# Kernel tuning notes

Hardware: AMD Instinct MI355X
Metric: run time of the kernel (lower is better)

The kernel has to match this reference:

```python
import jax, jax.numpy as jnp
import numpy as np
import math

D_MODEL = 2048
K = 64
W = 512              # window_size
STRIDE = W // 2      # = 256
EMA_ALPHA = 0.9
N_RETRIEVE = 8
EPS = 1e-12


def _build_cheby(k, w):
    # cheby_mat[k, n] = cos(k * arccos(t_n)), t_n = cos(pi*(2n+1)/(2w))
    ns = np.arange(w, dtype=np.float64)
    t = np.cos(np.pi * (2 * ns + 1) / (2 * w))
    ks = np.arange(k, dtype=np.float64)
    return jnp.asarray(np.cos(ks[:, None] * np.arccos(t)[None, :]), dtype=jnp.float32)


def setup_inputs() -> dict:
    key = jax.random.key(0)
    ks = jax.random.split(key, 5)
    B, S = 2, 8192
    scan_out = jax.random.normal(ks[0], (B, S, D_MODEL), dtype=jnp.float32)
    buf = jax.random.normal(ks[1], (W, D_MODEL), dtype=jnp.float32)  # pre-filled circular buffer
    # unit-modulus random-phase complex roles: r_k[d] = exp(i*theta)
    phases = jax.random.uniform(ks[2], (K, D_MODEL), dtype=jnp.float32) * (2.0 * math.pi)
    roles_real = jnp.cos(phases)
    roles_imag = jnp.sin(phases)
    w_bands = 1.0 / (jnp.arange(K, dtype=jnp.float32) + 1.0)  # w_init = 1/(k+1)
    retrieve_proj_w = jax.random.normal(ks[3], (D_MODEL, D_MODEL), dtype=jnp.float32) * 0.02
    inject_gate = jnp.zeros((1,), dtype=jnp.float32)
    cheby_mat = _build_cheby(K, W)
    return dict(scan_out=scan_out, buf=buf, roles_real=roles_real, roles_imag=roles_imag,
                w_bands=w_bands, retrieve_proj_w=retrieve_proj_w, inject_gate=inject_gate,
                cheby_mat=cheby_mat)


def reference(scan_out, buf, roles_real, roles_imag, w_bands, retrieve_proj_w, inject_gate, cheby_mat):
    S = scan_out.shape[1]
    h_mean = scan_out.mean(axis=0)                      # [S, D] batch-mean like torch code
    n_chunks = S // STRIDE
    chunks = h_mean.reshape(n_chunks, STRIDE, D_MODEL)  # each chunk triggers one bind

    init = (buf, jnp.int32(0),
            jnp.zeros((K, D_MODEL), jnp.float32),   # c_past
            jnp.zeros((D_MODEL,), jnp.float32),     # V_mem_real
            jnp.zeros((D_MODEL,), jnp.float32),     # V_mem_imag
            jnp.zeros((K,), jnp.float32),           # _coeff_norms (EMA)
            jnp.zeros((K,), jnp.float32))           # spectral_delta

    def step(carry, chunk):
        b, pos, c_past, vr, vi, cnorms, _ = carry
        # circular-buffer write of `stride` tokens starting at pos
        b = jax.lax.dynamic_update_slice(b, chunk, (pos, 0))
        pos = (pos + STRIDE) % W
        order = (jnp.arange(W, dtype=jnp.int32) + pos) % W   # oldest-first reorder
        data = b[order]                                      # [W, D]
        # Chebyshev coefficients: c = (2/W) * cheby_mat @ data, c0 halved
        coeffs = (2.0 / W) * (cheby_mat @ data)              # [K, D]
        coeffs = coeffs.at[0].multiply(0.5)
        # HRR-normalized bind into holographic memory via EMA
        norms = jnp.maximum(jnp.linalg.norm(coeffs, axis=-1, keepdims=True), EPS)
        cn = coeffs / norms
        cnorms = EMA_ALPHA * cnorms + (1.0 - EMA_ALPHA) * norms[:, 0]
        vr = EMA_ALPHA * vr + (1.0 - EMA_ALPHA) * (cn * roles_real).sum(axis=0)
        vi = EMA_ALPHA * vi + (1.0 - EMA_ALPHA) * (cn * roles_imag).sum(axis=0)
        # spectral delta vs previous window's coefficients
        delta = jnp.linalg.norm(coeffs - c_past, axis=-1)    # [K]
        return (b, pos, coeffs, vr, vi, cnorms, delta), None

    (b, pos, c_now, vr, vi, cnorms, delta), _ = jax.lax.scan(step, init, chunks)

    # retrieve: unbind top-J bands by spectral delta, denormalize, weight, project
    _, top = jax.lax.top_k(delta, N_RETRIEVE)                # [J]
    rr = roles_real[top]
    ri = roles_imag[top]
    retrieved = (vr[None, :] * rr + vi[None, :] * ri) * jnp.maximum(cnorms[top], EPS)[:, None]  # [J, D]
    weights = jax.nn.softplus(w_bands[top])                  # [J]
    ctx = (weights[:, None] * retrieved).sum(axis=0)         # [D]
    out = (ctx @ retrieve_proj_w.T) * jax.nn.sigmoid(inject_gate[0])  # [D]
    return out, delta, vr, vi
```

## Files before the change

kernel.cpp:

```cpp
#include <hip/hip_runtime.h>
#include <math.h>

#define D_MODEL 2048
#define KB_ 64
#define NCHUNK 32

typedef __bf16 bf16;
typedef __attribute__((ext_vector_type(8))) __bf16 bf16x8;
typedef __attribute__((ext_vector_type(4))) __bf16 bf16x4;
typedef __attribute__((ext_vector_type(4))) float f32x4;

#define OFF_COEFFS 0
#define OFF_NSQ    (32 * 64 * 2048)
#define OFF_NORMS  (OFF_NSQ + 32 * 64 * 32)
#define OFF_VR     (OFF_NORMS + 2048)
#define OFF_VI     (OFF_VR + 2048)
#define OFF_DSQ    (OFF_VI + 2048)

__device__ __forceinline__ void load_stage(
    const float* __restrict__ scan, const float* __restrict__ buf,
    int c, int nb, int n0, int dcol, float4* ra, float4* rb)
{
  if (c == 0 && nb < 4) {
    const float* bp = buf + (256 + nb * 64 + n0) * 2048 + dcol;
#pragma unroll
    for (int i = 0; i < 4; ++i) { ra[i] = *(const float4*)(bp + i * 2048); rb[i] = ra[i]; }
  } else {
    const float* p0 = scan + (c * 256 - 256 + nb * 64 + n0) * 2048 + dcol;
    const float* p1 = p0 + 8192 * 2048;
#pragma unroll
    for (int i = 0; i < 4; ++i) {
      ra[i] = *(const float4*)(p0 + i * 2048);
      rb[i] = *(const float4*)(p1 + i * 2048);
    }
  }
}

__device__ __forceinline__ void store_stage(
    bf16* Bsbuf, int n0, int d4, const float4* ra, const float4* rb)
{
  float4 m0 = make_float4(0.5f * (ra[0].x + rb[0].x), 0.5f * (ra[0].y + rb[0].y),
                          0.5f * (ra[0].z + rb[0].z), 0.5f * (ra[0].w + rb[0].w));
  float4 m1 = make_float4(0.5f * (ra[1].x + rb[1].x), 0.5f * (ra[1].y + rb[1].y),
                          0.5f * (ra[1].z + rb[1].z), 0.5f * (ra[1].w + rb[1].w));
  float4 m2 = make_float4(0.5f * (ra[2].x + rb[2].x), 0.5f * (ra[2].y + rb[2].y),
                          0.5f * (ra[2].z + rb[2].z), 0.5f * (ra[2].w + rb[2].w));
  float4 m3 = make_float4(0.5f * (ra[3].x + rb[3].x), 0.5f * (ra[3].y + rb[3].y),
                          0.5f * (ra[3].z + rb[3].z), 0.5f * (ra[3].w + rb[3].w));
  bf16x4 e0 = {(bf16)m0.x, (bf16)m1.x, (bf16)m2.x, (bf16)m3.x};
  bf16x4 e1 = {(bf16)m0.y, (bf16)m1.y, (bf16)m2.y, (bf16)m3.y};
  bf16x4 e2 = {(bf16)m0.z, (bf16)m1.z, (bf16)m2.z, (bf16)m3.z};
  bf16x4 e3 = {(bf16)m0.w, (bf16)m1.w, (bf16)m2.w, (bf16)m3.w};
  *(bf16x4*)(Bsbuf + (d4 + 0) * 72 + n0) = e0;
  *(bf16x4*)(Bsbuf + (d4 + 1) * 72 + n0) = e1;
  *(bf16x4*)(Bsbuf + (d4 + 2) * 72 + n0) = e2;
  *(bf16x4*)(Bsbuf + (d4 + 3) * 72 + n0) = e3;
}

__global__ __launch_bounds__(256, 4) void k1_fused(
    const float* __restrict__ scan, const float* __restrict__ buf,
    const float* __restrict__ cheby, float* __restrict__ coeffs,
    float* __restrict__ nsq, float* __restrict__ vzero)
{
  __shared__ bf16 Bs[2][64 * 72];

  const int t = threadIdx.x;
  const int dt = blockIdx.x;
  const int c  = blockIdx.y;
  const int w = t >> 6, lane = t & 63;
  const int quad = lane >> 4, r16 = lane & 15;
  const int d0 = dt * 64;
  const int n0 = (t >> 4) * 4;
  const int d4 = (t & 15) * 4;
  const int dcol = d0 + d4;

  if (dt == 0 && c == 0) {
    for (int i = t; i < 4160; i += 256) vzero[i] = 0.f;
  }

  f32x4 acc[4];
#pragma unroll
  for (int tn = 0; tn < 4; ++tn) acc[tn] = (f32x4){0.f, 0.f, 0.f, 0.f};

  float4 ra[4], rb[4];
  load_stage(scan, buf, c, 0, n0, dcol, ra, rb);
  store_stage(Bs[0], n0, d4, ra, rb);
  __syncthreads();

  for (int nb = 0; nb < 8; ++nb) {
    if (nb < 7) load_stage(scan, buf, c, nb + 1, n0, dcol, ra, rb);

    const float* ab = cheby + (w * 16 + r16) * 512 + nb * 64 + quad * 8;
    float4 f0 = *(const float4*)(ab);
    float4 f1 = *(const float4*)(ab + 4);
    float4 f2 = *(const float4*)(ab + 32);
    float4 f3 = *(const float4*)(ab + 36);
    bf16x8 a0 = {(bf16)f0.x, (bf16)f0.y, (bf16)f0.z, (bf16)f0.w,
                 (bf16)f1.x, (bf16)f1.y, (bf16)f1.z, (bf16)f1.w};
    bf16x8 a1 = {(bf16)f2.x, (bf16)f2.y, (bf16)f2.z, (bf16)f2.w,
                 (bf16)f3.x, (bf16)f3.y, (bf16)f3.z, (bf16)f3.w};

    const bf16* bsr = Bs[nb & 1];
#pragma unroll
    for (int ks = 0; ks < 2; ++ks) {
      bf16x8 a = ks ? a1 : a0;
#pragma unroll
      for (int tn = 0; tn < 4; ++tn) {
        bf16x8 bfr = *(const bf16x8*)(bsr + (tn * 16 + r16) * 72 + ks * 32 + quad * 8);
        acc[tn] = __builtin_amdgcn_mfma_f32_16x16x32_bf16(a, bfr, acc[tn], 0, 0, 0);
      }
    }

    if (nb < 7) store_stage(Bs[(nb + 1) & 1], n0, d4, ra, rb);
    __syncthreads();
  }

  const float scale = 2.0f / 512.0f;
  float sq[4] = {0.f, 0.f, 0.f, 0.f};
#pragma unroll
  for (int tn = 0; tn < 4; ++tn) {
#pragma unroll
    for (int rq = 0; rq < 4; ++rq) {
      int band = w * 16 + quad * 4 + rq;
      float sc = (band == 0) ? scale * 0.5f : scale;
      float v = acc[tn][rq] * sc;
      coeffs[(c * 64 + band) * 2048 + d0 + tn * 16 + r16] = v;
      sq[rq] += v * v;
    }
  }
#pragma unroll
  for (int off = 8; off > 0; off >>= 1) {
#pragma unroll
    for (int rq = 0; rq < 4; ++rq) sq[rq] += __shfl_down(sq[rq], off);
  }
  if (r16 == 0) {
#pragma unroll
    for (int rq = 0; rq < 4; ++rq)
      nsq[(c * 64 + w * 16 + quad * 4 + rq) * 32 + dt] = sq[rq];
  }
}

__global__ __launch_bounds__(256) void k2_bind(
    const float* __restrict__ coeffs, const float* __restrict__ nsq,
    const float* __restrict__ rr, const float* __restrict__ ri,
    float* __restrict__ vr, float* __restrict__ vi,
    float* __restrict__ dsq, float* __restrict__ norms)
{
  __shared__ float inv_s[16];
  const int t = threadIdx.x, lane = t & 63;
  const int xi = blockIdx.x >> 2, kg = blockIdx.x & 3;
  const int c = blockIdx.y;
  if (t < 16) {
    int k = kg * 16 + t;
    float s = 0.f;
#pragma unroll
    for (int dtile = 0; dtile < 32; ++dtile) s += nsq[(c * 64 + k) * 32 + dtile];
    float nrm = fmaxf(sqrtf(s), 1e-12f);
    inv_s[t] = 1.0f / nrm;
    if (xi == 0) norms[c * 64 + k] = nrm;
  }
  __syncthreads();
  const int d = xi * 256 + t;
  const float wc = 0.1f * powf(0.9f, (float)(31 - c));
  float ar = 0.f, ai = 0.f;
  if (c == 31) {
    for (int kk = 0; kk < 16; ++kk) {
      int k = kg * 16 + kk;
      float cf = coeffs[(31 * 64 + k) * 2048 + d];
      float cn = cf * inv_s[kk];
      ar += cn * rr[k * 2048 + d];
      ai += cn * ri[k * 2048 + d];
      float diff = cf - coeffs[(30 * 64 + k) * 2048 + d];
      float sqv = diff * diff;
#pragma unroll
      for (int o = 32; o > 0; o >>= 1) sqv += __shfl_down(sqv, o, 64);
      if (lane == 0) atomicAdd(&dsq[k], sqv);
    }
  } else {
    for (int kk = 0; kk < 16; ++kk) {
      int k = kg * 16 + kk;
      float cn = coeffs[(c * 64 + k) * 2048 + d] * inv_s[kk];
      ar += cn * rr[k * 2048 + d];
      ai += cn * ri[k * 2048 + d];
    }
  }
  atomicAdd(&vr[d], wc * ar);
  atomicAdd(&vi[d], wc * ai);
}

__global__ __launch_bounds__(256) void k4_gemv(
    const float* __restrict__ Wp, const float* __restrict__ norms,
    const float* __restrict__ dsq, const float* __restrict__ wb,
    const float* __restrict__ vr, const float* __restrict__ vi,
    const float* __restrict__ rr, const float* __restrict__ ri,
    const float* __restrict__ gate, float* __restrict__ dout)
{
  __shared__ float ctx_s[2048];
  __shared__ float cn_s[64];
  __shared__ int top_s[8];
  __shared__ float wgt_s[8];
  const int tid = threadIdx.x;
  const int lane = tid & 63;
  const int w = tid >> 6;

  if (tid < 64) {
    float s = 0.f;
    for (int c = 0; c < NCHUNK; ++c) s = 0.9f * s + 0.1f * norms[c * 64 + tid];
    cn_s[tid] = fmaxf(s, 1e-12f);
    if (blockIdx.x == 0) dout[D_MODEL + tid] = sqrtf(dsq[tid]);
  }
  if (tid == 0) {
    unsigned long long taken = 0ULL;
    for (int jj = 0; jj < 8; ++jj) {
      float best = -1.f;
      int bi = 0;
      for (int k = 0; k < 64; ++k) {
        float dv = dsq[k];
        if (!((taken >> k) & 1ULL) && dv > best) { best = dv; bi = k; }
      }
      taken |= (1ULL << bi);
      top_s[jj] = bi;
      wgt_s[jj] = log1pf(expf(wb[bi]));
    }
  }
  __syncthreads();

  {
    const int d8 = tid * 8;
#pragma unroll
    for (int h = 0; h < 2; ++h) {
      const int d = d8 + h * 4;
      float4 v_r = *(const float4*)(vr + d);
      float4 v_i = *(const float4*)(vi + d);
      float4 cx = make_float4(0.f, 0.f, 0.f, 0.f);
#pragma unroll
      for (int jj = 0; jj < 8; ++jj) {
        int k = top_s[jj];
        float g = wgt_s[jj] * cn_s[k];
        float4 r = *(const float4*)(rr + k * D_MODEL + d);
        float4 im = *(const float4*)(ri + k * D_MODEL + d);
        cx.x += g * (v_r.x * r.x + v_i.x * im.x);
        cx.y += g * (v_r.y * r.y + v_i.y * im.y);
        cx.z += g * (v_r.z * r.z + v_i.z * im.z);
        cx.w += g * (v_r.w * r.w + v_i.w * im.w);
      }
      *(float4*)(ctx_s + d) = cx;
    }
  }
  if (blockIdx.x < 8) {
    const int d = blockIdx.x * 256 + tid;
    dout[D_MODEL + KB_ + d] = vr[d];
    dout[D_MODEL + KB_ + D_MODEL + d] = vi[d];
  }
  __syncthreads();

  const int row = blockIdx.x * 4 + w;
  const float* p = Wp + row * D_MODEL;
  float s = 0.f;
#pragma unroll
  for (int i = 0; i < 8; ++i) {
    int e = lane * 4 + i * 256;
    float4 wv = *(const float4*)(p + e);
    float4 cv = *(const float4*)(ctx_s + e);
    s += wv.x * cv.x + wv.y * cv.y + wv.z * cv.z + wv.w * cv.w;
  }
#pragma unroll
  for (int o = 32; o > 0; o >>= 1) s += __shfl_down(s, o, 64);
  if (lane == 0) {
    float sig = 1.f / (1.f + expf(-gate[0]));
    dout[row] = s * sig;
  }
}

extern "C" void kernel_launch(void* const* d_in, const int* in_sizes, int n_in,
                              void* d_out, int out_size, void* d_ws, size_t ws_size,
                              hipStream_t stream) {
  const float* scan  = (const float*)d_in[0];
  const float* buf   = (const float*)d_in[1];
  const float* rr    = (const float*)d_in[2];
  const float* ri    = (const float*)d_in[3];
  const float* wb    = (const float*)d_in[4];
  const float* Wp    = (const float*)d_in[5];
  const float* gate  = (const float*)d_in[6];
  const float* cheby = (const float*)d_in[7];
  float* out = (float*)d_out;
  float* ws = (float*)d_ws;

  float* coeffs = ws + OFF_COEFFS;
  float* nsq    = ws + OFF_NSQ;
  float* norms  = ws + OFF_NORMS;
  float* vr     = ws + OFF_VR;
  float* vi     = ws + OFF_VI;
  float* dsq    = ws + OFF_DSQ;

  k1_fused<<<dim3(32, 32), 256, 0, stream>>>(scan, buf, cheby, coeffs, nsq, vr);
  k2_bind<<<dim3(32, 32), 256, 0, stream>>>(coeffs, nsq, rr, ri, vr, vi, dsq, norms);
  k4_gemv<<<512, 256, 0, stream>>>(Wp, norms, dsq, wb, vr, vi, rr, ri, gate, out);
}
```

Baseline: 273.4 us.

## Read each scan stride once and split overlapping-window projections into partials plus merge

Each 256-token stride was loaded twice, because consecutive 512-token windows overlap by half. Now each block loads one stride and projects it against both Chebyshev column halves. The results are written as two partial coefficient buffers, and a new merge kernel adds them and computes band norms, which replaces the old nsq partial-sum path. This roughly halves the reads of the large scan input, at the cost of extra partial writes and reads and one more kernel launch. The k2 inner loops are also unrolled.

```diff
diff --git a/kernel.cpp b/kernel.cpp
--- a/kernel.cpp
+++ b/kernel.cpp
@@ -10,23 +10,24 @@
 typedef __attribute__((ext_vector_type(4))) __bf16 bf16x4;
 typedef __attribute__((ext_vector_type(4))) float f32x4;
 
-#define OFF_COEFFS 0
-#define OFF_NSQ    (32 * 64 * 2048)
-#define OFF_NORMS  (OFF_NSQ + 32 * 64 * 32)
+#define OFF_S      0
+#define OFF_F      (32 * 64 * 2048)
+#define OFF_C      (2 * 32 * 64 * 2048)
+#define OFF_NORMS  (3 * 32 * 64 * 2048)
 #define OFF_VR     (OFF_NORMS + 2048)
 #define OFF_VI     (OFF_VR + 2048)
 #define OFF_DSQ    (OFF_VI + 2048)
 
 __device__ __forceinline__ void load_stage(
     const float* __restrict__ scan, const float* __restrict__ buf,
-    int c, int nb, int n0, int dcol, float4* ra, float4* rb)
-{
-  if (c == 0 && nb < 4) {
+    int j, int nb, int n0, int dcol, float4* ra, float4* rb)
+{
+  if (j == 32) {
     const float* bp = buf + (256 + nb * 64 + n0) * 2048 + dcol;
 #pragma unroll
     for (int i = 0; i < 4; ++i) { ra[i] = *(const float4*)(bp + i * 2048); rb[i] = ra[i]; }
   } else {
-    const float* p0 = scan + (c * 256 - 256 + nb * 64 + n0) * 2048 + dcol;
+    const float* p0 = scan + (j * 256 + nb * 64 + n0) * 2048 + dcol;
     const float* p1 = p0 + 8192 * 2048;
 #pragma unroll
     for (int i = 0; i < 4; ++i) {
@@ -57,16 +58,16 @@
   *(bf16x4*)(Bsbuf + (d4 + 3) * 72 + n0) = e3;
 }
 
-__global__ __launch_bounds__(256, 4) void k1_fused(
+__global__ __launch_bounds__(256, 4) void k1_part(
     const float* __restrict__ scan, const float* __restrict__ buf,
-    const float* __restrict__ cheby, float* __restrict__ coeffs,
-    float* __restrict__ nsq, float* __restrict__ vzero)
+    const float* __restrict__ cheby, float* __restrict__ bufS,
+    float* __restrict__ bufF, float* __restrict__ vzero)
 {
   __shared__ bf16 Bs[2][64 * 72];
 
   const int t = threadIdx.x;
   const int dt = blockIdx.x;
-  const int c  = blockIdx.y;
+  const int j  = blockIdx.y;
   const int w = t >> 6, lane = t & 63;
   const int quad = lane >> 4, r16 = lane & 15;
   const int d0 = dt * 64;
@@ -74,96 +75,116 @@
   const int d4 = (t & 15) * 4;
   const int dcol = d0 + d4;
 
-  if (dt == 0 && c == 0) {
+  if (dt == 0 && j == 0) {
     for (int i = t; i < 4160; i += 256) vzero[i] = 0.f;
   }
 
-  f32x4 acc[4];
-#pragma unroll
-  for (int tn = 0; tn < 4; ++tn) acc[tn] = (f32x4){0.f, 0.f, 0.f, 0.f};
+  f32x4 accS[4], accF[4];
+#pragma unroll
+  for (int tn = 0; tn < 4; ++tn) {
+    accS[tn] = (f32x4){0.f, 0.f, 0.f, 0.f};
+    accF[tn] = (f32x4){0.f, 0.f, 0.f, 0.f};
+  }
 
   float4 ra[4], rb[4];
-  load_stage(scan, buf, c, 0, n0, dcol, ra, rb);
+  load_stage(scan, buf, j, 0, n0, dcol, ra, rb);
   store_stage(Bs[0], n0, d4, ra, rb);
   __syncthreads();
 
-  for (int nb = 0; nb < 8; ++nb) {
-    if (nb < 7) load_stage(scan, buf, c, nb + 1, n0, dcol, ra, rb);
+  for (int nb = 0; nb < 4; ++nb) {
+    if (nb < 3) load_stage(scan, buf, j, nb + 1, n0, dcol, ra, rb);
 
     const float* ab = cheby + (w * 16 + r16) * 512 + nb * 64 + quad * 8;
     float4 f0 = *(const float4*)(ab);
     float4 f1 = *(const float4*)(ab + 4);
     float4 f2 = *(const float4*)(ab + 32);
     float4 f3 = *(const float4*)(ab + 36);
-    bf16x8 a0 = {(bf16)f0.x, (bf16)f0.y, (bf16)f0.z, (bf16)f0.w,
-                 (bf16)f1.x, (bf16)f1.y, (bf16)f1.z, (bf16)f1.w};
-    bf16x8 a1 = {(bf16)f2.x, (bf16)f2.y, (bf16)f2.z, (bf16)f2.w,
-                 (bf16)f3.x, (bf16)f3.y, (bf16)f3.z, (bf16)f3.w};
+    float4 g0 = *(const float4*)(ab + 256);
+    float4 g1 = *(const float4*)(ab + 260);
+    float4 g2 = *(const float4*)(ab + 288);
+    float4 g3 = *(const float4*)(ab + 292);
+    bf16x8 aF[2] = {{(bf16)f0.x, (bf16)f0.y, (bf16)f0.z, (bf16)f0.w,
+                     (bf16)f1.x, (bf16)f1.y, (bf16)f1.z, (bf16)f1.w},
+                    {(bf16)f2.x, (bf16)f2.y, (bf16)f2.z, (bf16)f2.w,
+                     (bf16)f3.x, (bf16)f3.y, (bf16)f3.z, (bf16)f3.w}};
+    bf16x8 aS[2] = {{(bf16)g0.x, (bf16)g0.y, (bf16)g0.z, (bf16)g0.w,
+                     (bf16)g1.x, (bf16)g1.y, (bf16)g1.z, (bf16)g1.w},
+                    {(bf16)g2.x, (bf16)g2.y, (bf16)g2.z, (bf16)g2.w,
+                     (bf16)g3.x, (bf16)g3.y, (bf16)g3.z, (bf16)g3.w}};
 
     const bf16* bsr = Bs[nb & 1];
 #pragma unroll
     for (int ks = 0; ks < 2; ++ks) {
-      bf16x8 a = ks ? a1 : a0;
 #pragma unroll
       for (int tn = 0; tn < 4; ++tn) {
         bf16x8 bfr = *(const bf16x8*)(bsr + (tn * 16 + r16) * 72 + ks * 32 + quad * 8);
-        acc[tn] = __builtin_amdgcn_mfma_f32_16x16x32_bf16(a, bfr, acc[tn], 0, 0, 0);
+        accS[tn] = __builtin_amdgcn_mfma_f32_16x16x32_bf16(aS[ks], bfr, accS[tn], 0, 0, 0);
+        accF[tn] = __builtin_amdgcn_mfma_f32_16x16x32_bf16(aF[ks], bfr, accF[tn], 0, 0, 0);
       }
     }
 
-    if (nb < 7) store_stage(Bs[(nb + 1) & 1], n0, d4, ra, rb);
+    if (nb < 3) store_stage(Bs[(nb + 1) & 1], n0, d4, ra, rb);
     __syncthreads();
   }
 
   const float scale = 2.0f / 512.0f;
-  float sq[4] = {0.f, 0.f, 0.f, 0.f};
+  const int jF = (j == 32) ? 0 : j + 1;
 #pragma unroll
   for (int tn = 0; tn < 4; ++tn) {
 #pragma unroll
     for (int rq = 0; rq < 4; ++rq) {
       int band = w * 16 + quad * 4 + rq;
       float sc = (band == 0) ? scale * 0.5f : scale;
-      float v = acc[tn][rq] * sc;
-      coeffs[(c * 64 + band) * 2048 + d0 + tn * 16 + r16] = v;
-      sq[rq] += v * v;
-    }
-  }
-#pragma unroll
-  for (int off = 8; off > 0; off >>= 1) {
-#pragma unroll
-    for (int rq = 0; rq < 4; ++rq) sq[rq] += __shfl_down(sq[rq], off);
-  }
-  if (r16 == 0) {
-#pragma unroll
-    for (int rq = 0; rq < 4; ++rq)
-      nsq[(c * 64 + w * 16 + quad * 4 + rq) * 32 + dt] = sq[rq];
-  }
+      int dd = d0 + tn * 16 + r16;
+      if (j < 32) bufS[(j * 64 + band) * 2048 + dd] = accS[tn][rq] * sc;
+      if (j != 31) bufF[(jF * 64 + band) * 2048 + dd] = accF[tn][rq] * sc;
+    }
+  }
+}
+
+__global__ __launch_bounds__(256) void k1m_merge(
+    const float* __restrict__ bufS, const float* __restrict__ bufF,
+    float* __restrict__ coeffs, float* __restrict__ norms)
+{
+  const int t = threadIdx.x, lane = t & 63, wv = t >> 6;
+  const int kq = blockIdx.x;
+  const int c  = blockIdx.y;
+  const int k  = kq * 4 + wv;
+  const float* ps = bufS + (c * 64 + k) * 2048;
+  const float* pf = bufF + (c * 64 + k) * 2048;
+  float*       pc = coeffs + (c * 64 + k) * 2048;
+  float ssum = 0.f;
+#pragma unroll
+  for (int i = 0; i < 8; ++i) {
+    int d = lane * 4 + i * 256;
+    float4 s = *(const float4*)(ps + d);
+    float4 f = *(const float4*)(pf + d);
+    float4 m = make_float4(s.x + f.x, s.y + f.y, s.z + f.z, s.w + f.w);
+    *(float4*)(pc + d) = m;
+    ssum += m.x * m.x + m.y * m.y + m.z * m.z + m.w * m.w;
+  }
+#pragma unroll
+  for (int o = 32; o > 0; o >>= 1) ssum += __shfl_down(ssum, o, 64);
+  if (lane == 0) norms[c * 64 + k] = fmaxf(sqrtf(ssum), 1e-12f);
 }
 
 __global__ __launch_bounds__(256) void k2_bind(
-    const float* __restrict__ coeffs, const float* __restrict__ nsq,
+    const float* __restrict__ coeffs, const float* __restrict__ norms,
     const float* __restrict__ rr, const float* __restrict__ ri,
     float* __restrict__ vr, float* __restrict__ vi,
-    float* __restrict__ dsq, float* __restrict__ norms)
+    float* __restrict__ dsq)
 {
   __shared__ float inv_s[16];
   const int t = threadIdx.x, lane = t & 63;
   const int xi = blockIdx.x >> 2, kg = blockIdx.x & 3;
   const int c = blockIdx.y;
-  if (t < 16) {
-    int k = kg * 16 + t;
-    float s = 0.f;
-#pragma unroll
-    for (int dtile = 0; dtile < 32; ++dtile) s += nsq[(c * 64 + k) * 32 + dtile];
-    float nrm = fmaxf(sqrtf(s), 1e-12f);
-    inv_s[t] = 1.0f / nrm;
-    if (xi == 0) norms[c * 64 + k] = nrm;
-  }
+  if (t < 16) inv_s[t] = 1.0f / norms[c * 64 + kg * 16 + t];
   __syncthreads();
   const int d = xi * 256 + t;
   const float wc = 0.1f * powf(0.9f, (float)(31 - c));
   float ar = 0.f, ai = 0.f;
   if (c == 31) {
+#pragma unroll
     for (int kk = 0; kk < 16; ++kk) {
       int k = kg * 16 + kk;
       float cf = coeffs[(31 * 64 + k) * 2048 + d];
@@ -177,6 +198,7 @@
       if (lane == 0) atomicAdd(&dsq[k], sqv);
     }
   } else {
+#pragma unroll
     for (int kk = 0; kk < 16; ++kk) {
       int k = kg * 16 + kk;
       float cn = coeffs[(c * 64 + k) * 2048 + d] * inv_s[kk];
@@ -286,14 +308,16 @@
   float* out = (float*)d_out;
   float* ws = (float*)d_ws;
 
-  float* coeffs = ws + OFF_COEFFS;
-  float* nsq    = ws + OFF_NSQ;
+  float* bufS   = ws + OFF_S;
+  float* bufF   = ws + OFF_F;
+  float* coeffs = ws + OFF_C;
   float* norms  = ws + OFF_NORMS;
   float* vr     = ws + OFF_VR;
   float* vi     = ws + OFF_VI;
   float* dsq    = ws + OFF_DSQ;
 
-  k1_fused<<<dim3(32, 32), 256, 0, stream>>>(scan, buf, cheby, coeffs, nsq, vr);
-  k2_bind<<<dim3(32, 32), 256, 0, stream>>>(coeffs, nsq, rr, ri, vr, vi, dsq, norms);
+  k1_part<<<dim3(32, 33), 256, 0, stream>>>(scan, buf, cheby, bufS, bufF, vr);
+  k1m_merge<<<dim3(16, 32), 256, 0, stream>>>(bufS, bufF, coeffs, norms);
+  k2_bind<<<dim3(32, 32), 256, 0, stream>>>(coeffs, norms, rr, ri, vr, vi, dsq);
   k4_gemv<<<512, 256, 0, stream>>>(Wp, norms, dsq, wb, vr, vi, rr, ri, gate, out);
 }
```

Measured after the change: 281.3 us. +2.9%, slower.
